# Kernel tuning notes

Measured on AMD Instinct MI355X. Metric: run time of the kernel, lower is better.

The kernel has to match this reference:

```python
import jax, jax.numpy as jnp
import numpy as np

# Dims (match init_kwargs config)
D_L, D_A, D_V = 300, 74, 35
DH_L, DH_A, DH_V = 512, 256, 256
MEM = 512
H_MLP = 1024          # h_att1 = h_att2 = h_gamma1 = h_gamma2 = h_out
T, N = 64, 1024
TOTAL_H = DH_L + DH_A + DH_V          # 1024
ATT_IN = 2 * TOTAL_H                  # 2048 (windowsize=2)
GAMMA_IN = ATT_IN + MEM               # 2560
FINAL = TOTAL_H + MEM                 # 1536


def setup_inputs() -> dict:
    key = jax.random.key(0)
    ks = iter(jax.random.split(key, 64))
    def p(shape):
        return jax.random.normal(next(ks), shape, jnp.float32) * 0.05
    inp = {
        "x": jax.random.normal(next(ks), (T, N, D_L + D_A + D_V), jnp.float32),
        "h_l_prior": jnp.zeros((N, DH_L), jnp.float32),
        "h_a_prior": jnp.zeros((N, DH_A), jnp.float32),
        "h_v_prior": jnp.zeros((N, DH_V), jnp.float32),
        "mem_prior": jnp.zeros((N, MEM), jnp.float32),
        # LSTMCell params (torch layout: W_ih [4H, In], gate order i,f,g,o)
        "W_ih_l": p((4 * DH_L, D_L)), "W_hh_l": p((4 * DH_L, DH_L)),
        "b_ih_l": p((4 * DH_L,)), "b_hh_l": p((4 * DH_L,)),
        "W_ih_a": p((4 * DH_A, D_A)), "W_hh_a": p((4 * DH_A, DH_A)),
        "b_ih_a": p((4 * DH_A,)), "b_hh_a": p((4 * DH_A,)),
        "W_ih_v": p((4 * DH_V, D_V)), "W_hh_v": p((4 * DH_V, DH_V)),
        "b_ih_v": p((4 * DH_V,)), "b_hh_v": p((4 * DH_V,)),
        # attention / gamma / out MLPs (torch Linear: weight [out, in])
        "att1_w1": p((H_MLP, ATT_IN)), "att1_b1": p((H_MLP,)),
        "att1_w2": p((ATT_IN, H_MLP)), "att1_b2": p((ATT_IN,)),
        "att2_w1": p((H_MLP, ATT_IN)), "att2_b1": p((H_MLP,)),
        "att2_w2": p((MEM, H_MLP)), "att2_b2": p((MEM,)),
        "g1_w1": p((H_MLP, GAMMA_IN)), "g1_b1": p((H_MLP,)),
        "g1_w2": p((MEM, H_MLP)), "g1_b2": p((MEM,)),
        "g2_w1": p((H_MLP, GAMMA_IN)), "g2_b1": p((H_MLP,)),
        "g2_w2": p((MEM, H_MLP)), "g2_b2": p((MEM,)),
        "out_w1": p((H_MLP, FINAL)), "out_b1": p((H_MLP,)),
        "out_w2": p((1, H_MLP)), "out_b2": p((1,)),
    }
    return inp


def _lstm_cell(xt, h, c, Wih, Whh, bih, bhh):
    g = xt @ Wih.T + bih + h @ Whh.T + bhh
    i, f, gg, o = jnp.split(g, 4, axis=1)
    c2 = jax.nn.sigmoid(f) * c + jax.nn.sigmoid(i) * jnp.tanh(gg)
    h2 = jax.nn.sigmoid(o) * jnp.tanh(c2)
    return h2, c2


def _mlp2(z, w1, b1, w2, b2):
    # fc2(relu(fc1(z))); dropout is identity at inference
    return jax.nn.relu(z @ w1.T + b1) @ w2.T + b2


def reference(x, h_l_prior, h_a_prior, h_v_prior, mem_prior,
              W_ih_l, W_hh_l, b_ih_l, b_hh_l,
              W_ih_a, W_hh_a, b_ih_a, b_hh_a,
              W_ih_v, W_hh_v, b_ih_v, b_hh_v,
              att1_w1, att1_b1, att1_w2, att1_b2,
              att2_w1, att2_b1, att2_w2, att2_b2,
              g1_w1, g1_b1, g1_w2, g1_b2,
              g2_w1, g2_b1, g2_w2, g2_b2,
              out_w1, out_b1, out_w2, out_b2):
    n = x.shape[1]
    x_l = x[:, :, :D_L]
    x_a = x[:, :, D_L:D_L + D_A]
    x_v = x[:, :, D_L + D_A:]
    # states are re-initialized to zeros (priors unused, as in original forward)
    z = lambda d: jnp.zeros((n, d), x.dtype)
    carry = (z(DH_L), z(DH_L), z(DH_A), z(DH_A), z(DH_V), z(DH_V), z(MEM))

    def step(carry, xs):
        h_l, c_l, h_a, c_a, h_v, c_v, mem = carry
        xl, xa, xv = xs
        nh_l, nc_l = _lstm_cell(xl, h_l, c_l, W_ih_l, W_hh_l, b_ih_l, b_hh_l)
        nh_a, nc_a = _lstm_cell(xa, h_a, c_a, W_ih_a, W_hh_a, b_ih_a, b_hh_a)
        nh_v, nc_v = _lstm_cell(xv, h_v, c_v, W_ih_v, W_hh_v, b_ih_v, b_hh_v)
        # cStar = [prev_cs, new_cs]  -> [n, 2*TOTAL_H]
        cStar = jnp.concatenate([c_l, c_a, c_v, nc_l, nc_a, nc_v], axis=1)
        att = jax.nn.softmax(_mlp2(cStar, att1_w1, att1_b1, att1_w2, att1_b2), axis=1)
        attended = att * cStar
        cHat = jnp.tanh(_mlp2(attended, att2_w1, att2_b1, att2_w2, att2_b2))
        both = jnp.concatenate([attended, mem], axis=1)
        gamma1 = jax.nn.sigmoid(_mlp2(both, g1_w1, g1_b1, g1_w2, g1_b2))
        gamma2 = jax.nn.sigmoid(_mlp2(both, g2_w1, g2_b1, g2_w2, g2_b2))
        mem2 = gamma1 * mem + gamma2 * cHat
        return (nh_l, nc_l, nh_a, nc_a, nh_v, nc_v, mem2), None

    (h_l, c_l, h_a, c_a, h_v, c_v, mem), _ = jax.lax.scan(step, carry, (x_l, x_a, x_v))
    last_hs = jnp.concatenate([h_l, h_a, h_v, mem], axis=1)  # [n, FINAL]
    return _mlp2(last_hs, out_w1, out_b1, out_w2, out_b2)     # [n, 1]
```

## Files before the change

### kernel.cpp

```cpp
#include <hip/hip_runtime.h>
#include <hip/hip_bf16.h>

typedef unsigned short u16;
typedef unsigned int   u32;
typedef __attribute__((ext_vector_type(8))) short s16x8;
typedef __attribute__((ext_vector_type(4))) float f32x4;

#define NB   1024
#define TT   64
#define DXL  300
#define DXA  74
#define DXV  35
#define DX   (DXL+DXA+DXV)
#define DHL  512
#define DHA  256
#define DHV  256
#define TOTH 1024
#define MEMD 512
#define HMLP 1024
#define ATTIN 2048
#define GAMIN 2560
#define PXL  320
#define PXA  128
#define PXV  64

__device__ __forceinline__ u16 f2b(float f) {
    union { float f; u32 u; } x; x.f = f;
    u32 r = x.u + 0x7fffu + ((x.u >> 16) & 1u);
    return (u16)(r >> 16);
}

__device__ __forceinline__ void gload_lds16(const void* g, void* l) {
    __builtin_amdgcn_global_load_lds(
        (const __attribute__((address_space(1))) unsigned int*)g,
        (__attribute__((address_space(3))) unsigned int*)l,
        16, 0, 0);
}

struct GP {
    const u16* A0; const u16* A1; const u16* Wpk;
    const float* b0; const float* b1; void* C;
    int lda0, K0, lda1, K1, ldc, act, outbf, bStart, gx;
};

__global__ __launch_bounds__(256, 8) void gemm_group(GP p0, GP p1, GP p2,
                                                     GP p3, GP p4, GP p5)
{
    __shared__ u16 As[2][64 * 64];
    GP p;
    {
        int bx = blockIdx.x;
        if      (bx >= p5.bStart) p = p5;
        else if (bx >= p4.bStart) p = p4;
        else if (bx >= p3.bStart) p = p3;
        else if (bx >= p2.bStart) p = p2;
        else if (bx >= p1.bStart) p = p1;
        else                      p = p0;
    }
    const int tid  = threadIdx.x;
    const int wid  = tid >> 6;
    const int lane = tid & 63;
    const int local = blockIdx.x - p.bStart;
    const int by   = local / p.gx;
    const int bm   = by * 64;
    const int ntile= local - by * p.gx;
    const int bn   = ntile * 64;
    const int wr = wid >> 1, wc = wid & 1;
    const int nt = (p.K0 + p.K1) >> 6;
    const int e0 = wid * 128 + lane;

    auto stageA = [&](int t, int buf) {
        int k0 = t << 6;
        const u16* Ap; int ldA, ka;
        if (k0 < p.K0) { Ap = p.A0; ldA = p.lda0; ka = k0; }
        else           { Ap = p.A1; ldA = p.lda1; ka = k0 - p.K0; }
        #pragma unroll
        for (int i = 0; i < 2; ++i) {
            int e   = e0 + i * 64;
            int row = e >> 3;
            int c   = (e & 7) ^ (row & 7);
            gload_lds16(Ap + (size_t)(bm + row) * ldA + ka + c * 8,
                        (char*)&As[buf][0] + (wid * 2 + i) * 1024);
        }
    };

    f32x4 acc[2][2] = {};
    stageA(0, 0);
    __syncthreads();

    const u16* wbase = p.Wpk + ((size_t)ntile * nt << 12) + (wc << 11) + lane * 8;

    for (int t = 0; t < nt; ++t) {
        if (t + 1 < nt) stageA(t + 1, (t + 1) & 1);
        const char* Ab = (const char*)&As[t & 1][0];
        const u16* wt  = wbase + ((size_t)t << 12);
        #pragma unroll
        for (int ks = 0; ks < 2; ++ks) {
            s16x8 af[2], bf[2];
            const int ca = ks * 4 + (lane >> 4);
            #pragma unroll
            for (int f = 0; f < 2; ++f) {
                int ra = wr * 32 + f * 16 + (lane & 15);
                af[f] = *(const s16x8*)(Ab + ra * 128 + ((ca ^ (ra & 7))) * 16);
                bf[f] = *(const s16x8*)(wt + (ks << 10) + (f << 9));
            }
            #pragma unroll
            for (int fi = 0; fi < 2; ++fi)
                #pragma unroll
                for (int fj = 0; fj < 2; ++fj)
                    acc[fi][fj] = __builtin_amdgcn_mfma_f32_16x16x32_bf16(
                        af[fi], bf[fj], acc[fi][fj], 0, 0, 0);
        }
        __syncthreads();
    }

    #pragma unroll
    for (int fi = 0; fi < 2; ++fi)
        #pragma unroll
        for (int fj = 0; fj < 2; ++fj) {
            int col = bn + wc * 32 + fj * 16 + (lane & 15);
            float bia = p.b0[col];
            if (p.b1) bia += p.b1[col];
            #pragma unroll
            for (int r4 = 0; r4 < 4; ++r4) {
                int row = bm + wr * 32 + fi * 16 + (lane >> 4) * 4 + r4;
                float v = acc[fi][fj][r4] + bia;
                if (p.act == 1)      v = fmaxf(v, 0.f);
                else if (p.act == 2) v = 1.f / (1.f + __expf(-v));
                else if (p.act == 3) v = tanhf(v);
                if (p.outbf) ((u16*)p.C)[(size_t)row * p.ldc + col] = f2b(v);
                else         ((float*)p.C)[(size_t)row * p.ldc + col] = v;
            }
        }
}

__device__ __forceinline__ void lstm_elem(
    const float* __restrict__ gl, const float* __restrict__ ga,
    const float* __restrict__ gv, const float* __restrict__ cs_prev,
    float* __restrict__ cs_new, u16* __restrict__ cs_new_b,
    u16* __restrict__ hs_new_b, int idx)
{
    int n = idx >> 10, u = idx & 1023;
    const float* g; int dh, gu;
    if (u < DHL)            { g = gl; dh = DHL; gu = u; }
    else if (u < DHL + DHA) { g = ga; dh = DHA; gu = u - DHL; }
    else                    { g = gv; dh = DHV; gu = u - DHL - DHA; }
    const float* grow = g + (size_t)n * 4 * dh;
    float gi = grow[gu], gf = grow[dh + gu], gg = grow[2 * dh + gu], go = grow[3 * dh + gu];
    float c  = cs_prev[idx];
    float si = 1.f / (1.f + __expf(-gi));
    float sf = 1.f / (1.f + __expf(-gf));
    float so = 1.f / (1.f + __expf(-go));
    float c2 = sf * c + si * tanhf(gg);
    float h2 = so * tanhf(c2);
    cs_new[idx]   = c2;
    cs_new_b[idx] = f2b(c2);
    hs_new_b[idx] = f2b(h2);
}

__device__ __forceinline__ void xcvt_elem(
    const float* __restrict__ X, int t, int n, int u,
    u16* __restrict__ xl, u16* __restrict__ xa, u16* __restrict__ xv)
{
    const float* row = X + ((size_t)t * NB + n) * DX;
    if (u < PXL)            xl[n * PXL + u] = f2b(u < DXL ? row[u] : 0.f);
    else if (u < PXL + PXA) { int q = u - PXL;       xa[n * PXA + q] = f2b(q < DXA ? row[DXL + q] : 0.f); }
    else                    { int q = u - PXL - PXA; xv[n * PXV + q] = f2b(q < DXV ? row[DXL + DXA + q] : 0.f); }
}

__global__ void lstm_pointwise(const float* __restrict__ gl,
                               const float* __restrict__ ga,
                               const float* __restrict__ gv,
                               const float* __restrict__ cs_prev,
                               float* __restrict__ cs_new,
                               u16* __restrict__ cs_new_b,
                               u16* __restrict__ hs_new_b,
                               const float* __restrict__ X, int tnext,
                               u16* __restrict__ xl, u16* __restrict__ xa,
                               u16* __restrict__ xv)
{
    int idx = blockIdx.x * blockDim.x + threadIdx.x;
    if (idx >= NB * TOTH) return;
    lstm_elem(gl, ga, gv, cs_prev, cs_new, cs_new_b, hs_new_b, idx);
    int n = idx >> 10, u = idx & 1023;
    if (tnext < TT && u < 512) xcvt_elem(X, tnext, n, u, xl, xa, xv);
}

__global__ __launch_bounds__(256) void fused_mid(
    const float* __restrict__ logits,
    const float* __restrict__ csP,
    const float* __restrict__ csN,
    u16* __restrict__ attended_b,
    int do_mem,
    float* __restrict__ memb, u16* __restrict__ membb,
    const float* __restrict__ g1, const float* __restrict__ g2,
    const float* __restrict__ chat,
    int do_pw,
    const float* __restrict__ gl, const float* __restrict__ ga,
    const float* __restrict__ gv,
    float* __restrict__ pw_cs_new,
    u16* __restrict__ pw_cs_new_b,
    u16* __restrict__ pw_hs_new_b,
    const float* __restrict__ X, int tnext,
    u16* __restrict__ xl, u16* __restrict__ xa, u16* __restrict__ xv)
{
    int n = blockIdx.x;
    int tid = threadIdx.x, lane = tid & 63, wid = tid >> 6;

    if (do_mem) {
        for (int k = tid; k < MEMD; k += 256) {
            size_t i = (size_t)n * MEMD + k;
            float v = g1[i] * memb[i] + g2[i] * chat[i];
            memb[i]  = v;
            membb[i] = f2b(v);
        }
    }

    const float* z = logits + (size_t)n * ATTIN;
    __shared__ float sred[4];

    float m = -1e30f;
    for (int k = tid; k < ATTIN; k += 256) m = fmaxf(m, z[k]);
    #pragma unroll
    for (int off = 1; off < 64; off <<= 1) m = fmaxf(m, __shfl_xor(m, off));
    if (lane == 0) sred[wid] = m;
    __syncthreads();
    m = fmaxf(fmaxf(sred[0], sred[1]), fmaxf(sred[2], sred[3]));
    __syncthreads();

    float s = 0.f;
    for (int k = tid; k < ATTIN; k += 256) s += __expf(z[k] - m);
    #pragma unroll
    for (int off = 1; off < 64; off <<= 1) s += __shfl_xor(s, off);
    if (lane == 0) sred[wid] = s;
    __syncthreads();
    s = sred[0] + sred[1] + sred[2] + sred[3];
    float inv = 1.f / s;

    for (int k = tid; k < ATTIN; k += 256) {
        float cs = (k < TOTH) ? csP[(size_t)n * TOTH + k]
                              : csN[(size_t)n * TOTH + (k - TOTH)];
        attended_b[(size_t)n * ATTIN + k] = f2b(__expf(z[k] - m) * inv * cs);
    }

    if (do_pw) {
        __syncthreads();
        #pragma unroll
        for (int j = 0; j < 4; ++j) {
            int u = tid + j * 256;
            lstm_elem(gl, ga, gv, csN, pw_cs_new, pw_cs_new_b, pw_hs_new_b,
                      n * 1024 + u);
        }
        if (tnext < TT) {
            #pragma unroll
            for (int j = 0; j < 2; ++j) {
                int u = tid + j * 256;
                xcvt_elem(X, tnext, n, u, xl, xa, xv);
            }
        }
    }
}

__global__ void mem_update(float* __restrict__ memb,
                           u16* __restrict__ memb_b,
                           const float* __restrict__ g1,
                           const float* __restrict__ g2,
                           const float* __restrict__ chat)
{
    int idx = blockIdx.x * blockDim.x + threadIdx.x;
    if (idx >= NB * MEMD) return;
    float v = g1[idx] * memb[idx] + g2[idx] * chat[idx];
    memb[idx]   = v;
    memb_b[idx] = f2b(v);
}

__global__ __launch_bounds__(256) void out_dot(const float* __restrict__ hid,
                                               const float* __restrict__ w2,
                                               const float* __restrict__ b2,
                                               float* __restrict__ out)
{
    int wid = threadIdx.x >> 6, lane = threadIdx.x & 63;
    int n = blockIdx.x * 4 + wid;
    if (n >= NB) return;
    const float* h = hid + (size_t)n * HMLP;
    float s = 0.f;
    for (int k = lane; k < HMLP; k += 64) s += h[k] * w2[k];
    #pragma unroll
    for (int off = 1; off < 64; off <<= 1) s += __shfl_xor(s, off);
    if (lane == 0) out[n] = s + b2[0];
}

__global__ void cvt_x(const float* __restrict__ X,
                      u16* __restrict__ xl, u16* __restrict__ xa, u16* __restrict__ xv,
                      int t)
{
    int idx = blockIdx.x * blockDim.x + threadIdx.x;
    if (idx >= NB * 512) return;
    xcvt_elem(X, t, idx >> 9, idx & 511, xl, xa, xv);
}

__global__ void concat2(const float* __restrict__ a, const float* __restrict__ b,
                        float* __restrict__ d)
{
    int i = blockIdx.x * 256 + threadIdx.x;
    if (i < 1024)      d[i] = a[i];
    else if (i < 2048) d[i] = b[i - 1024];
}

#define NPK 12
struct PK {
    const float* s0; int ld0, k0src, k0;
    const float* s1; int ld1, k1src;
    u16* dst; int ntiles, ktot, bstart;
};
struct PKPack { PK d[NPK]; };

__global__ __launch_bounds__(256) void wpack_all(PKPack wp)
{
    int bx = blockIdx.x;
    int di = 0;
    #pragma unroll
    for (int i = 1; i < NPK; ++i) if (bx >= wp.d[i].bstart) di = i;
    PK d = wp.d[di];
    int NT = d.ktot >> 6;
    int total8 = d.ntiles * 8 * d.ktot;
    int g = (bx - d.bstart) * 256 + threadIdx.x;
    if (g >= total8) return;
    int lane = g & 63;
    int fj   = (g >> 6) & 1;
    int ks   = (g >> 7) & 1;
    int wc   = (g >> 8) & 1;
    int rest = g >> 9;
    int t    = rest % NT;
    int ntile= rest / NT;
    int row  = ntile * 64 + wc * 32 + fj * 16 + (lane & 15);
    int kb   = t * 64 + ks * 32 + (lane >> 4) * 8;
    u16* o = d.dst + (size_t)g * 8;
    #pragma unroll
    for (int j = 0; j < 8; ++j) {
        int k = kb + j;
        float v;
        if (k < d.k0) v = (k < d.k0src) ? d.s0[(size_t)row * d.ld0 + k] : 0.f;
        else { int kk = k - d.k0; v = (kk < d.k1src) ? d.s1[(size_t)row * d.ld1 + kk] : 0.f; }
        o[j] = f2b(v);
    }
}

__global__ void fill0(u32* __restrict__ p, int n)
{
    int i = blockIdx.x * blockDim.x + threadIdx.x;
    if (i < n) p[i] = 0u;
}

static GP mkgp(const u16* A0, int lda0, int K0, const u16* A1, int lda1, int K1,
               const u16* Wpk, const float* b0, const float* b1,
               void* C, int ldc, int Nout, int act, int outbf)
{
    GP p;
    p.A0 = A0; p.A1 = A1; p.Wpk = Wpk; p.b0 = b0; p.b1 = b1; p.C = C;
    p.lda0 = lda0; p.K0 = K0; p.lda1 = lda1; p.K1 = K1;
    p.ldc = ldc; p.act = act; p.outbf = outbf;
    p.bStart = 0; p.gx = Nout / 64;
    return p;
}

static void launch_group(hipStream_t s, GP* p, int np)
{
    int total = 0;
    for (int i = 0; i < np; ++i) { p[i].bStart = total; total += p[i].gx * 16; }
    GP dummy = {};
    dummy.bStart = 0x7fffffff;
    GP a1 = (np > 1) ? p[1] : dummy;
    GP a2 = (np > 2) ? p[2] : dummy;
    GP a3 = (np > 3) ? p[3] : dummy;
    GP a4 = (np > 4) ? p[4] : dummy;
    GP a5 = (np > 5) ? p[5] : dummy;
    gemm_group<<<dim3(total), 256, 0, s>>>(p[0], a1, a2, a3, a4, a5);
}

extern "C" void kernel_launch(void* const* d_in, const int* in_sizes, int n_in,
                              void* d_out, int out_size, void* d_ws, size_t ws_size,
                              hipStream_t stream)
{
    const float* X     = (const float*)d_in[0];
    const float* Wih_l = (const float*)d_in[5];
    const float* Whh_l = (const float*)d_in[6];
    const float* bih_l = (const float*)d_in[7];
    const float* bhh_l = (const float*)d_in[8];
    const float* Wih_a = (const float*)d_in[9];
    const float* Whh_a = (const float*)d_in[10];
    const float* bih_a = (const float*)d_in[11];
    const float* bhh_a = (const float*)d_in[12];
    const float* Wih_v = (const float*)d_in[13];
    const float* Whh_v = (const float*)d_in[14];
    const float* bih_v = (const float*)d_in[15];
    const float* bhh_v = (const float*)d_in[16];
    const float* a1w1  = (const float*)d_in[17];
    const float* a1b1  = (const float*)d_in[18];
    const float* a1w2  = (const float*)d_in[19];
    const float* a1b2  = (const float*)d_in[20];
    const float* a2w1  = (const float*)d_in[21];
    const float* a2b1  = (const float*)d_in[22];
    const float* a2w2  = (const float*)d_in[23];
    const float* a2b2  = (const float*)d_in[24];
    const float* g1w1  = (const float*)d_in[25];
    const float* g1b1  = (const float*)d_in[26];
    const float* g1w2  = (const float*)d_in[27];
    const float* g1b2  = (const float*)d_in[28];
    const float* g2w1  = (const float*)d_in[29];
    const float* g2b1  = (const float*)d_in[30];
    const float* g2w2  = (const float*)d_in[31];
    const float* g2b2  = (const float*)d_in[32];
    const float* ow1   = (const float*)d_in[33];
    const float* ob1   = (const float*)d_in[34];
    const float* ow2   = (const float*)d_in[35];
    const float* ob2   = (const float*)d_in[36];
    float* out = (float*)d_out;

    char* wsp = (char*)d_ws;
    auto take = [&](size_t bytes) -> char* {
        char* r = wsp; wsp += (bytes + 255) & ~(size_t)255; return r;
    };
    float* cs0  = (float*)take((size_t)NB * TOTH * 4);
    float* cs1  = (float*)take((size_t)NB * TOTH * 4);
    float* memb = (float*)take((size_t)NB * MEMD * 4);
    float* gl   = (float*)take((size_t)NB * 2048 * 4);
    float* ga   = (float*)take((size_t)NB * 1024 * 4);
    float* gv   = (float*)take((size_t)NB * 1024 * 4);
    float* lgts = (float*)take((size_t)NB * ATTIN * 4);
    float* chat = (float*)take((size_t)NB * MEMD * 4);
    float* gm1  = (float*)take((size_t)NB * MEMD * 4);
    float* gm2  = (float*)take((size_t)NB * MEMD * 4);
    float* hout = (float*)take((size_t)NB * HMLP * 4);
    float* cb2  = (float*)take((size_t)2048 * 4);
    u16* hs0b  = (u16*)take((size_t)NB * TOTH * 2);
    u16* hs1b  = (u16*)take((size_t)NB * TOTH * 2);
    u16* cs0b  = (u16*)take((size_t)NB * TOTH * 2);
    u16* cs1b  = (u16*)take((size_t)NB * TOTH * 2);
    u16* membb = (u16*)take((size_t)NB * MEMD * 2);
    u16* xlb   = (u16*)take((size_t)NB * PXL * 2);
    u16* xab   = (u16*)take((size_t)NB * PXA * 2);
    u16* xvb   = (u16*)take((size_t)NB * PXV * 2);
    u16* hid1b = (u16*)take((size_t)NB * HMLP * 2);
    u16* hcat  = (u16*)take((size_t)NB * 3072 * 2);
    u16* attdb = (u16*)take((size_t)NB * ATTIN * 2);
    u16* lpk    = (u16*)take((size_t)2048 * 832 * 2);
    u16* apk    = (u16*)take((size_t)1024 * 384 * 2);
    u16* vpk    = (u16*)take((size_t)1024 * 320 * 2);
    u16* a1w1pk = (u16*)take((size_t)1024 * 2048 * 2);
    u16* a1w2pk = (u16*)take((size_t)2048 * 1024 * 2);
    u16* a2w1pk = (u16*)take((size_t)1024 * 2048 * 2);
    u16* g12pk  = (u16*)take((size_t)2048 * 2560 * 2);
    u16* a2w2pk = (u16*)take((size_t)512 * 1024 * 2);
    u16* g1w2pk = (u16*)take((size_t)512 * 1024 * 2);
    u16* g2w2pk = (u16*)take((size_t)512 * 1024 * 2);
    u16* ow1pk  = (u16*)take((size_t)1024 * 1536 * 2);

    {
        int nf = NB * (TOTH * 2 + MEMD);
        fill0<<<(nf + 255) / 256, 256, 0, stream>>>((u32*)cs0, nf);
        int nb = NB * (TOTH * 4 + MEMD) / 2;
        fill0<<<(nb + 255) / 256, 256, 0, stream>>>((u32*)hs0b, nb);
    }
    {
        PKPack wp;
        PK descs[NPK] = {
            { Wih_l, DXL, DXL, PXL,  Whh_l, DHL, DHL,  lpk,    32, 832,  0 },
            { Wih_a, DXA, DXA, PXA,  Whh_a, DHA, DHA,  apk,    16, 384,  0 },
            { Wih_v, DXV, DXV, PXV,  Whh_v, DHV, DHV,  vpk,    16, 320,  0 },
            { a1w1, ATTIN, ATTIN, ATTIN, nullptr, 0, 0, a1w1pk, 16, 2048, 0 },
            { a1w2, HMLP, HMLP, HMLP,    nullptr, 0, 0, a1w2pk, 32, 1024, 0 },
            { a2w1, ATTIN, ATTIN, ATTIN, nullptr, 0, 0, a2w1pk, 16, 2048, 0 },
            { g1w1, GAMIN, GAMIN, GAMIN, nullptr, 0, 0, g12pk,  16, 2560, 0 },
            { g2w1, GAMIN, GAMIN, GAMIN, nullptr, 0, 0, g12pk + (size_t)1024 * 2560, 16, 2560, 0 },
            { a2w2, HMLP, HMLP, HMLP,    nullptr, 0, 0, a2w2pk,  8, 1024, 0 },
            { g1w2, HMLP, HMLP, HMLP,    nullptr, 0, 0, g1w2pk,  8, 1024, 0 },
            { g2w2, HMLP, HMLP, HMLP,    nullptr, 0, 0, g2w2pk,  8, 1024, 0 },
            { ow1,  1536, 1536, 1536,    nullptr, 0, 0, ow1pk,  16, 1536, 0 },
        };
        int total = 0;
        for (int i = 0; i < NPK; ++i) {
            descs[i].bstart = total;
            int groups = descs[i].ntiles * 8 * descs[i].ktot;
            total += (groups + 255) / 256;
            wp.d[i] = descs[i];
        }
        wpack_all<<<total, 256, 0, stream>>>(wp);
    }
    concat2<<<8, 256, 0, stream>>>(g1b1, g2b1, cb2);
    cvt_x<<<(NB * 512 + 255) / 256, 256, 0, stream>>>(X, xlb, xab, xvb, 0);

    float* csf[2] = { cs0, cs1 };
    u16*   csb[2] = { cs0b, cs1b };
    u16*   hsb[2] = { hs0b, hs1b };

    {
        GP ps[3] = {
            mkgp(xlb, PXL, PXL, hsb[0], TOTH, DHL, lpk, bih_l, bhh_l, gl, 2048, 2048, 0, 0),
            mkgp(xab, PXA, PXA, hsb[0] + DHL, TOTH, DHA, apk, bih_a, bhh_a, ga, 1024, 1024, 0, 0),
            mkgp(xvb, PXV, PXV, hsb[0] + DHL + DHA, TOTH, DHV, vpk, bih_v, bhh_v, gv, 1024, 1024, 0, 0) };
        launch_group(stream, ps, 3);
    }
    lstm_pointwise<<<(NB * TOTH + 255) / 256, 256, 0, stream>>>(
        gl, ga, gv, csf[0], csf[1], csb[1], hsb[1], X, 1, xlb, xab, xvb);
    {
        GP ps[4] = {
            mkgp(csb[0], TOTH, TOTH, csb[1], TOTH, TOTH, a1w1pk, a1b1, nullptr,
                 hid1b, HMLP, HMLP, 1, 1),
            mkgp(xlb, PXL, PXL, hsb[1], TOTH, DHL, lpk, bih_l, bhh_l, gl, 2048, 2048, 0, 0),
            mkgp(xab, PXA, PXA, hsb[1] + DHL, TOTH, DHA, apk, bih_a, bhh_a, ga, 1024, 1024, 0, 0),
            mkgp(xvb, PXV, PXV, hsb[1] + DHL + DHA, TOTH, DHV, vpk, bih_v, bhh_v, gv, 1024, 1024, 0, 0) };
        launch_group(stream, ps, 4);
    }
    {
        GP ps[1] = { mkgp(hid1b, HMLP, HMLP, nullptr, 0, 0, a1w2pk, a1b2, nullptr,
                          lgts, ATTIN, ATTIN, 0, 0) };
        launch_group(stream, ps, 1);
    }

    for (int t = 0; t < TT; ++t) {
        fused_mid<<<NB, 256, 0, stream>>>(
            lgts, csf[t & 1], csf[(t + 1) & 1], attdb,
            t > 0 ? 1 : 0, memb, membb, gm1, gm2, chat,
            t < TT - 1 ? 1 : 0, gl, ga, gv,
            csf[t & 1], csb[t & 1], hsb[t & 1],
            X, t + 2, xlb, xab, xvb);

        {
            GP ps[6]; int np = 0;
            ps[np++] = mkgp(attdb, ATTIN, ATTIN, membb, MEMD, MEMD, g12pk, cb2, nullptr,
                            hcat + 1024, 3072, 2048, 1, 1);
            ps[np++] = mkgp(attdb, ATTIN, ATTIN, nullptr, 0, 0, a2w1pk, a2b1, nullptr,
                            hcat, 3072, 1024, 1, 1);
            if (t < TT - 1)
                ps[np++] = mkgp(csb[(t + 1) & 1], TOTH, TOTH, csb[t & 1], TOTH, TOTH,
                                a1w1pk, a1b1, nullptr, hid1b, HMLP, HMLP, 1, 1);
            if (t < TT - 2) {
                ps[np++] = mkgp(xlb, PXL, PXL, hsb[t & 1], TOTH, DHL, lpk,
                                bih_l, bhh_l, gl, 2048, 2048, 0, 0);
                ps[np++] = mkgp(xab, PXA, PXA, hsb[t & 1] + DHL, TOTH, DHA, apk,
                                bih_a, bhh_a, ga, 1024, 1024, 0, 0);
                ps[np++] = mkgp(xvb, PXV, PXV, hsb[t & 1] + DHL + DHA, TOTH, DHV, vpk,
                                bih_v, bhh_v, gv, 1024, 1024, 0, 0);
            }
            launch_group(stream, ps, np);
        }

        {
            GP ps[4]; int np = 0;
            if (t < TT - 1)
                ps[np++] = mkgp(hid1b, HMLP, HMLP, nullptr, 0, 0, a1w2pk, a1b2, nullptr,
                                lgts, ATTIN, ATTIN, 0, 0);
            ps[np++] = mkgp(hcat, 3072, HMLP, nullptr, 0, 0, a2w2pk, a2b2, nullptr,
                            chat, MEMD, MEMD, 3, 0);
            ps[np++] = mkgp(hcat + 1024, 3072, HMLP, nullptr, 0, 0, g1w2pk, g1b2, nullptr,
                            gm1, MEMD, MEMD, 2, 0);
            ps[np++] = mkgp(hcat + 2048, 3072, HMLP, nullptr, 0, 0, g2w2pk, g2b2, nullptr,
                            gm2, MEMD, MEMD, 2, 0);
            launch_group(stream, ps, np);
        }
    }

    mem_update<<<(NB * MEMD + 255) / 256, 256, 0, stream>>>(memb, membb, gm1, gm2, chat);
    {
        GP ps[1] = { mkgp(hsb[0], TOTH, TOTH, membb, MEMD, MEMD, ow1pk, ob1, nullptr,
                          hout, HMLP, HMLP, 1, 0) };
        launch_group(stream, ps, 1);
    }
    out_dot<<<NB / 4, 256, 0, stream>>>(hout, ow2, ob2, out);
}
```

Before: 5.424 ms.

## Load GEMM A tiles directly into registers with double-buffered prefetch, drop LDS

Replaces the LDS staging of A tiles (global_load_lds plus __syncthreads per k-step) with direct global-to-register loads of A and B fragments. Two register buffers are ping-ponged so the loads for the next k-tile are issued before the MFMAs of the current one. This removes LDS traffic and block barriers. In exchange, each A row is now fetched from global or L2 by both column waves, and register pressure rises, so launch bounds drop to 4 blocks per CU.

New measurement: 10.54 ms. 94.3% more time.

```diff
diff --git a/kernel.cpp b/kernel.cpp
--- a/kernel.cpp
+++ b/kernel.cpp
@@ -30,23 +30,27 @@
     return (u16)(r >> 16);
 }
 
-__device__ __forceinline__ void gload_lds16(const void* g, void* l) {
-    __builtin_amdgcn_global_load_lds(
-        (const __attribute__((address_space(1))) unsigned int*)g,
-        (__attribute__((address_space(3))) unsigned int*)l,
-        16, 0, 0);
-}
-
 struct GP {
     const u16* A0; const u16* A1; const u16* Wpk;
     const float* b0; const float* b1; void* C;
     int lda0, K0, lda1, K1, ldc, act, outbf, bStart, gx;
 };
 
-__global__ __launch_bounds__(256, 8) void gemm_group(GP p0, GP p1, GP p2,
+#define MFMA_STEP(af, bf)                                                     \
+    do {                                                                      \
+        _Pragma("unroll")                                                     \
+        for (int ks = 0; ks < 2; ++ks)                                        \
+            _Pragma("unroll")                                                 \
+            for (int fi = 0; fi < 2; ++fi)                                    \
+                _Pragma("unroll")                                             \
+                for (int fj = 0; fj < 2; ++fj)                                \
+                    acc[fi][fj] = __builtin_amdgcn_mfma_f32_16x16x32_bf16(    \
+                        af[ks * 2 + fi], bf[ks * 2 + fj], acc[fi][fj], 0, 0, 0); \
+    } while (0)
+
+__global__ __launch_bounds__(256, 4) void gemm_group(GP p0, GP p1, GP p2,
                                                      GP p3, GP p4, GP p5)
 {
-    __shared__ u16 As[2][64 * 64];
     GP p;
     {
         int bx = blockIdx.x;
@@ -67,52 +71,42 @@
     const int bn   = ntile * 64;
     const int wr = wid >> 1, wc = wid & 1;
     const int nt = (p.K0 + p.K1) >> 6;
-    const int e0 = wid * 128 + lane;
-
-    auto stageA = [&](int t, int buf) {
+
+    const u16* wbase = p.Wpk + ((size_t)ntile * nt << 12) + (wc << 11) + lane * 8;
+    const int ar0 = bm + wr * 32 + (lane & 15);
+    const int cchunk = (lane >> 4) * 8;
+
+    auto loadA = [&](int t, s16x8 (&af)[4]) {
         int k0 = t << 6;
         const u16* Ap; int ldA, ka;
         if (k0 < p.K0) { Ap = p.A0; ldA = p.lda0; ka = k0; }
         else           { Ap = p.A1; ldA = p.lda1; ka = k0 - p.K0; }
-        #pragma unroll
-        for (int i = 0; i < 2; ++i) {
-            int e   = e0 + i * 64;
-            int row = e >> 3;
-            int c   = (e & 7) ^ (row & 7);
-            gload_lds16(Ap + (size_t)(bm + row) * ldA + ka + c * 8,
-                        (char*)&As[buf][0] + (wid * 2 + i) * 1024);
-        }
+        const u16* r0 = Ap + (size_t)ar0 * ldA + ka + cchunk;
+        const u16* r1 = r0 + (size_t)16 * ldA;
+        af[0] = *(const s16x8*)(r0);
+        af[1] = *(const s16x8*)(r1);
+        af[2] = *(const s16x8*)(r0 + 32);
+        af[3] = *(const s16x8*)(r1 + 32);
     };
+    auto loadB = [&](int t, s16x8 (&bf)[4]) {
+        const u16* wt = wbase + ((size_t)t << 12);
+        bf[0] = *(const s16x8*)(wt);
+        bf[1] = *(const s16x8*)(wt + 512);
+        bf[2] = *(const s16x8*)(wt + 1024);
+        bf[3] = *(const s16x8*)(wt + 1536);
+    };
 
     f32x4 acc[2][2] = {};
-    stageA(0, 0);
-    __syncthreads();
-
-    const u16* wbase = p.Wpk + ((size_t)ntile * nt << 12) + (wc << 11) + lane * 8;
-
-    for (int t = 0; t < nt; ++t) {
-        if (t + 1 < nt) stageA(t + 1, (t + 1) & 1);
-        const char* Ab = (const char*)&As[t & 1][0];
-        const u16* wt  = wbase + ((size_t)t << 12);
-        #pragma unroll
-        for (int ks = 0; ks < 2; ++ks) {
-            s16x8 af[2], bf[2];
-            const int ca = ks * 4 + (lane >> 4);
-            #pragma unroll
-            for (int f = 0; f < 2; ++f) {
-                int ra = wr * 32 + f * 16 + (lane & 15);
-                af[f] = *(const s16x8*)(Ab + ra * 128 + ((ca ^ (ra & 7))) * 16);
-                bf[f] = *(const s16x8*)(wt + (ks << 10) + (f << 9));
-            }
-            #pragma unroll
-            for (int fi = 0; fi < 2; ++fi)
-                #pragma unroll
-                for (int fj = 0; fj < 2; ++fj)
-                    acc[fi][fj] = __builtin_amdgcn_mfma_f32_16x16x32_bf16(
-                        af[fi], bf[fj], acc[fi][fj], 0, 0, 0);
-        }
-        __syncthreads();
-    }
+    s16x8 aA[4], bA[4], aB[4], bB[4];
+    loadA(0, aA); loadB(0, bA);
+    int t = 0;
+    for (; t + 2 <= nt; t += 2) {
+        loadA(t + 1, aB); loadB(t + 1, bB);
+        MFMA_STEP(aA, bA);
+        if (t + 2 < nt) { loadA(t + 2, aA); loadB(t + 2, bA); }
+        MFMA_STEP(aB, bB);
+    }
+    if (t < nt) MFMA_STEP(aA, bA);
 
     #pragma unroll
     for (int fi = 0; fi < 2; ++fi)
```

## Double GEMM K-tile to 128 and pad LSTM inputs to match

Applied to the files above, without the earlier changes.

The grouped bf16 MFMA GEMM now stages a 64x128 A tile per iteration instead of 64x64. This halves the number of main-loop iterations and the barriers between them. Because every K segment must now be a multiple of 128, the L and V LSTM input paddings grow (320→384, 64→128) and the packed weight buffers and conversion kernels change to match. The cost is doubled LDS per block, which lowers the occupancy hint from 8 to 5. The padding also adds zero work to the LSTM input GEMMs.

Result: slower. 5.687 ms (+4.8%).

```diff
diff --git a/kernel.cpp b/kernel.cpp
--- a/kernel.cpp
+++ b/kernel.cpp
@@ -20,9 +20,10 @@
 #define HMLP 1024
 #define ATTIN 2048
 #define GAMIN 2560
-#define PXL  320
+#define PXL  384
 #define PXA  128
-#define PXV  64
+#define PXV  128
+#define PXT  (PXL+PXA+PXV)
 
 __device__ __forceinline__ u16 f2b(float f) {
     union { float f; u32 u; } x; x.f = f;
@@ -43,10 +44,10 @@
     int lda0, K0, lda1, K1, ldc, act, outbf, bStart, gx;
 };
 
-__global__ __launch_bounds__(256, 8) void gemm_group(GP p0, GP p1, GP p2,
+__global__ __launch_bounds__(256, 5) void gemm_group(GP p0, GP p1, GP p2,
                                                      GP p3, GP p4, GP p5)
 {
-    __shared__ u16 As[2][64 * 64];
+    __shared__ u16 As[2][64 * 128];
     GP p;
     {
         int bx = blockIdx.x;
@@ -66,50 +67,56 @@
     const int ntile= local - by * p.gx;
     const int bn   = ntile * 64;
     const int wr = wid >> 1, wc = wid & 1;
-    const int nt = (p.K0 + p.K1) >> 6;
-    const int e0 = wid * 128 + lane;
+    const int nt  = (p.K0 + p.K1) >> 7;
+    const int ntB = nt << 1;
 
     auto stageA = [&](int t, int buf) {
-        int k0 = t << 6;
+        int k0 = t << 7;
         const u16* Ap; int ldA, ka;
         if (k0 < p.K0) { Ap = p.A0; ldA = p.lda0; ka = k0; }
         else           { Ap = p.A1; ldA = p.lda1; ka = k0 - p.K0; }
         #pragma unroll
-        for (int i = 0; i < 2; ++i) {
-            int e   = e0 + i * 64;
-            int row = e >> 3;
-            int c   = (e & 7) ^ (row & 7);
-            gload_lds16(Ap + (size_t)(bm + row) * ldA + ka + c * 8,
-                        (char*)&As[buf][0] + (wid * 2 + i) * 1024);
-        }
+        for (int s = 0; s < 2; ++s)
+            #pragma unroll
+            for (int i = 0; i < 2; ++i) {
+                int e   = wid * 128 + i * 64 + lane;
+                int row = e >> 3;
+                int c   = (e & 7) ^ (row & 7);
+                gload_lds16(Ap + (size_t)(bm + row) * ldA + ka + s * 64 + c * 8,
+                            (char*)&As[buf][0] + s * 8192 + (wid * 2 + i) * 1024);
+            }
     };
 
     f32x4 acc[2][2] = {};
     stageA(0, 0);
     __syncthreads();
 
-    const u16* wbase = p.Wpk + ((size_t)ntile * nt << 12) + (wc << 11) + lane * 8;
+    const u16* wbase = p.Wpk + (((size_t)ntile * ntB) << 12) + (wc << 11) + lane * 8;
 
     for (int t = 0; t < nt; ++t) {
         if (t + 1 < nt) stageA(t + 1, (t + 1) & 1);
         const char* Ab = (const char*)&As[t & 1][0];
-        const u16* wt  = wbase + ((size_t)t << 12);
         #pragma unroll
-        for (int ks = 0; ks < 2; ++ks) {
-            s16x8 af[2], bf[2];
-            const int ca = ks * 4 + (lane >> 4);
+        for (int ss = 0; ss < 2; ++ss) {
+            const u16* wt = wbase + (((size_t)(2 * t + ss)) << 12);
             #pragma unroll
-            for (int f = 0; f < 2; ++f) {
-                int ra = wr * 32 + f * 16 + (lane & 15);
-                af[f] = *(const s16x8*)(Ab + ra * 128 + ((ca ^ (ra & 7))) * 16);
-                bf[f] = *(const s16x8*)(wt + (ks << 10) + (f << 9));
+            for (int ks = 0; ks < 2; ++ks) {
+                s16x8 af[2], bf[2];
+                const int ca = ks * 4 + (lane >> 4);
+                #pragma unroll
+                for (int f = 0; f < 2; ++f) {
+                    int ra = wr * 32 + f * 16 + (lane & 15);
+                    af[f] = *(const s16x8*)(Ab + ss * 8192 + ra * 128 +
+                                            ((ca ^ (ra & 7))) * 16);
+                    bf[f] = *(const s16x8*)(wt + (ks << 10) + (f << 9));
+                }
+                #pragma unroll
+                for (int fi = 0; fi < 2; ++fi)
+                    #pragma unroll
+                    for (int fj = 0; fj < 2; ++fj)
+                        acc[fi][fj] = __builtin_amdgcn_mfma_f32_16x16x32_bf16(
+                            af[fi], bf[fj], acc[fi][fj], 0, 0, 0);
             }
-            #pragma unroll
-            for (int fi = 0; fi < 2; ++fi)
-                #pragma unroll
-                for (int fj = 0; fj < 2; ++fj)
-                    acc[fi][fj] = __builtin_amdgcn_mfma_f32_16x16x32_bf16(
-                        af[fi], bf[fj], acc[fi][fj], 0, 0, 0);
         }
         __syncthreads();
     }
@@ -183,7 +190,7 @@
     if (idx >= NB * TOTH) return;
     lstm_elem(gl, ga, gv, cs_prev, cs_new, cs_new_b, hs_new_b, idx);
     int n = idx >> 10, u = idx & 1023;
-    if (tnext < TT && u < 512) xcvt_elem(X, tnext, n, u, xl, xa, xv);
+    if (tnext < TT && u < PXT) xcvt_elem(X, tnext, n, u, xl, xa, xv);
 }
 
 __global__ __launch_bounds__(256) void fused_mid(
@@ -253,9 +260,9 @@
         }
         if (tnext < TT) {
             #pragma unroll
-            for (int j = 0; j < 2; ++j) {
+            for (int j = 0; j < 3; ++j) {
                 int u = tid + j * 256;
-                xcvt_elem(X, tnext, n, u, xl, xa, xv);
+                if (u < PXT) xcvt_elem(X, tnext, n, u, xl, xa, xv);
             }
         }
     }
@@ -295,8 +302,9 @@
                       int t)
 {
     int idx = blockIdx.x * blockDim.x + threadIdx.x;
-    if (idx >= NB * 512) return;
-    xcvt_elem(X, t, idx >> 9, idx & 511, xl, xa, xv);
+    if (idx >= NB * PXT) return;
+    int n = idx / PXT, u = idx - n * PXT;
+    xcvt_elem(X, t, n, u, xl, xa, xv);
 }
 
 __global__ void concat2(const float* __restrict__ a, const float* __restrict__ b,
@@ -444,9 +452,9 @@
     u16* hid1b = (u16*)take((size_t)NB * HMLP * 2);
     u16* hcat  = (u16*)take((size_t)NB * 3072 * 2);
     u16* attdb = (u16*)take((size_t)NB * ATTIN * 2);
-    u16* lpk    = (u16*)take((size_t)2048 * 832 * 2);
+    u16* lpk    = (u16*)take((size_t)2048 * 896 * 2);
     u16* apk    = (u16*)take((size_t)1024 * 384 * 2);
-    u16* vpk    = (u16*)take((size_t)1024 * 320 * 2);
+    u16* vpk    = (u16*)take((size_t)1024 * 384 * 2);
     u16* a1w1pk = (u16*)take((size_t)1024 * 2048 * 2);
     u16* a1w2pk = (u16*)take((size_t)2048 * 1024 * 2);
     u16* a2w1pk = (u16*)take((size_t)1024 * 2048 * 2);
@@ -465,9 +473,9 @@
     {
         PKPack wp;
         PK descs[NPK] = {
-            { Wih_l, DXL, DXL, PXL,  Whh_l, DHL, DHL,  lpk,    32, 832,  0 },
+            { Wih_l, DXL, DXL, PXL,  Whh_l, DHL, DHL,  lpk,    32, 896,  0 },
             { Wih_a, DXA, DXA, PXA,  Whh_a, DHA, DHA,  apk,    16, 384,  0 },
-            { Wih_v, DXV, DXV, PXV,  Whh_v, DHV, DHV,  vpk,    16, 320,  0 },
+            { Wih_v, DXV, DXV, PXV,  Whh_v, DHV, DHV,  vpk,    16, 384,  0 },
             { a1w1, ATTIN, ATTIN, ATTIN, nullptr, 0, 0, a1w1pk, 16, 2048, 0 },
             { a1w2, HMLP, HMLP, HMLP,    nullptr, 0, 0, a1w2pk, 32, 1024, 0 },
             { a2w1, ATTIN, ATTIN, ATTIN, nullptr, 0, 0, a2w1pk, 16, 2048, 0 },
@@ -488,7 +496,7 @@
         wpack_all<<<total, 256, 0, stream>>>(wp);
     }
     concat2<<<8, 256, 0, stream>>>(g1b1, g2b1, cb2);
-    cvt_x<<<(NB * 512 + 255) / 256, 256, 0, stream>>>(X, xlb, xab, xvb, 0);
+    cvt_x<<<(NB * PXT + 255) / 256, 256, 0, stream>>>(X, xlb, xab, xvb, 0);
 
     float* csf[2] = { cs0, cs1 };
     u16*   csb[2] = { cs0b, cs1b };
```
